# Optimization experiments

Hardware: AMD Instinct MI355X
Metric: run time of the kernel (lower is better)

Reference implementation:

```python
import math
import jax, jax.numpy as jnp
import numpy as np

B, L, D, K = 4, 1024, 256, 64
PI = np.float32(math.pi)


def setup_inputs() -> dict:
    key = jax.random.key(0)
    ks = jax.random.split(key, 16)
    s = 0.05
    return {
        "x": jax.random.normal(ks[0], (B, L, D), jnp.float32),
        "pos_phases": jax.random.normal(ks[1], (L, K), jnp.float32) * PI,
        "W1": jax.random.normal(ks[2], (D, D), jnp.float32) * s,
        "b1": jnp.zeros((D,), jnp.float32),
        "W2": jax.random.normal(ks[3], (D, K), jnp.float32) * s,
        "b2": jnp.zeros((K,), jnp.float32),
        "Wa": jax.random.normal(ks[4], (D, K), jnp.float32) * s,
        "ba": jnp.zeros((K,), jnp.float32),
        "Wv": jax.random.normal(ks[5], (D, D), jnp.float32) * s,
        "bv": jnp.zeros((D,), jnp.float32),
        "ln_g": jnp.ones((D,), jnp.float32),
        "ln_b": jnp.zeros((D,), jnp.float32),
        "Wo": jax.random.normal(ks[6], (D, D), jnp.float32) * s,
        "bo": jnp.zeros((D,), jnp.float32),
    }


def reference(x, pos_phases, W1, b1, W2, b2, Wa, ba, Wv, bv, ln_g, ln_b, Wo, bo):
    b, l, d = x.shape
    k = Wa.shape[1]
    # content phase encoder: Linear -> GELU(exact) -> Linear, then tanh * pi
    h = jax.nn.gelu(x @ W1 + b1, approximate=False)
    content_phase = jnp.tanh(h @ W2 + b2) * PI                      # (B,L,K)
    phase = pos_phases[None, :l] + content_phase                    # (B,L,K)
    amp = jax.nn.softplus(x @ Wa + ba) + 0.1                        # (B,L,K)
    # phasor = amp * exp(i*phase), kept as real/imag parts
    pr = amp * jnp.cos(phase)
    pim = amp * jnp.sin(phase)
    V = x @ Wv + bv                                                 # (B,L,D)
    # bound = phasor[...,None] * V[...,None,:]; cumsum over L
    mr = jnp.cumsum(pr[..., None] * V[..., None, :], axis=1)        # (B,L,K,D)
    mi = jnp.cumsum(pim[..., None] * V[..., None, :], axis=1)       # (B,L,K,D)
    # Re(memory * conj(phasor)) summed over K
    retrieved = (jnp.einsum('blkd,blk->bld', mr, pr)
                 + jnp.einsum('blkd,blk->bld', mi, pim))            # (B,L,D)
    positions = jnp.arange(1, l + 1, dtype=x.dtype)
    norm = jnp.sqrt(positions * k)[None, :, None]
    r = retrieved / norm
    # to_out: LayerNorm then Linear
    mu = jnp.mean(r, axis=-1, keepdims=True)
    var = jnp.var(r, axis=-1, keepdims=True)
    rn = (r - mu) * jax.lax.rsqrt(var + 1e-5) * ln_g + ln_b
    return x + (rn @ Wo + bo)
```

## Files before the change

### kernel.cpp

```cpp
#include <hip/hip_runtime.h>
#include <hip/hip_bf16.h>
#include <math.h>

#define BB 4
#define LL 1024
#define DD 256
#define KK 64
#define NN (BB*LL)

typedef __attribute__((ext_vector_type(8))) short short8;
typedef __attribute__((ext_vector_type(4))) float f32x4;

__device__ __forceinline__ short f2bs(float f){
    union { __hip_bfloat16 h; short s; } u;
    u.h = __float2bfloat16(f);
    return u.s;
}

__global__ __launch_bounds__(256)
void prep_kernel(const float* __restrict__ x,
                 const float* __restrict__ W1, const float* __restrict__ Wv,
                 const float* __restrict__ Wo, const float* __restrict__ W2,
                 const float* __restrict__ Wa,
                 short* __restrict__ xb,
                 short* __restrict__ W1t, short* __restrict__ Wvt,
                 short* __restrict__ Wot, short* __restrict__ W2t,
                 short* __restrict__ Wat)
{
    int o = blockIdx.x * 256 + threadIdx.x;
    if (o < NN*DD){
        xb[o] = f2bs(x[o]);
        return;
    }
    o -= NN*DD;
    if (o < 3*DD*DD){
        int m = o / (DD*DD);
        int e = o - m*DD*DD;
        int n = e >> 8, k = e & 255;
        const float* src = (m==0) ? W1 : (m==1) ? Wv : Wo;
        short* dst = (m==0) ? W1t : (m==1) ? Wvt : Wot;
        dst[n*DD + k] = f2bs(src[k*DD + n]);
        return;
    }
    o -= 3*DD*DD;
    int m = o >> 14;
    int e = o & 16383;
    int n = e >> 8, k = e & 255;
    const float* src = (m==0) ? W2 : Wa;
    short* dst = (m==0) ? W2t : Wat;
    dst[n*DD + k] = f2bs(src[k*KK + n]);
}

__global__ __launch_bounds__(256)
void encode_kernel(const short* __restrict__ xb, const float* __restrict__ pos,
                   const short* __restrict__ W1t, const short* __restrict__ Wvt,
                   const short* __restrict__ W2t, const short* __restrict__ Wat,
                   const float* __restrict__ b1, const float* __restrict__ bv,
                   const float* __restrict__ b2, const float* __restrict__ ba,
                   short* __restrict__ Pb, short* __restrict__ Vb)
{
    const int t = threadIdx.x;
    const int w = t >> 6, lane = t & 63;
    const int m16 = lane & 15, quad = lane >> 4;
    const int tok0 = blockIdx.x * 16;

    __shared__ __align__(16) short hsb[16][264];

    short8 aX[8];
    {
        const short* xr = xb + (size_t)(tok0 + m16)*DD + quad*8;
        #pragma unroll
        for (int kk = 0; kk < 8; kk++) aX[kk] = *(const short8*)(xr + kk*32);
    }

    f32x4 accH[4], accV[4];
    #pragma unroll
    for (int i = 0; i < 4; i++){ accH[i] = (f32x4){0,0,0,0}; accV[i] = (f32x4){0,0,0,0}; }
    #pragma unroll
    for (int kk = 0; kk < 8; kk++){
        const short* p1 = W1t + (size_t)(w*64 + m16)*DD + kk*32 + quad*8;
        const short* pv = Wvt + (size_t)(w*64 + m16)*DD + kk*32 + quad*8;
        #pragma unroll
        for (int ns = 0; ns < 4; ns++){
            accH[ns] = __builtin_amdgcn_mfma_f32_16x16x32_bf16(
                           aX[kk], *(const short8*)(p1 + ns*16*DD), accH[ns], 0,0,0);
            accV[ns] = __builtin_amdgcn_mfma_f32_16x16x32_bf16(
                           aX[kk], *(const short8*)(pv + ns*16*DD), accV[ns], 0,0,0);
        }
    }
    #pragma unroll
    for (int ns = 0; ns < 4; ns++){
        int col = w*64 + ns*16 + m16;
        float bb1 = b1[col], bbv = bv[col];
        #pragma unroll
        for (int r2 = 0; r2 < 4; r2++){
            int row = quad*4 + r2;
            float hx = accH[ns][r2] + bb1;
            hsb[row][col] = f2bs(0.5f*hx*(1.0f + erff(hx*0.70710678118f)));
            Vb[(size_t)(tok0+row)*DD + col] = f2bs(accV[ns][r2] + bbv);
        }
    }
    __syncthreads();

    f32x4 accT = (f32x4){0,0,0,0}, accA = (f32x4){0,0,0,0};
    {
        const short* p2 = W2t + (size_t)(w*16 + m16)*DD + quad*8;
        const short* pa = Wat + (size_t)(w*16 + m16)*DD + quad*8;
        #pragma unroll
        for (int kk = 0; kk < 8; kk++){
            short8 aH = *(const short8*)&hsb[m16][kk*32 + quad*8];
            accT = __builtin_amdgcn_mfma_f32_16x16x32_bf16(
                       aH, *(const short8*)(p2 + kk*32), accT, 0,0,0);
            accA = __builtin_amdgcn_mfma_f32_16x16x32_bf16(
                       aX[kk], *(const short8*)(pa + kk*32), accA, 0,0,0);
        }
    }
    const int k = w*16 + m16;
    float bb2 = b2[k], bba = ba[k];
    const float PI_ = 3.14159265358979323846f;
    #pragma unroll
    for (int r2 = 0; r2 < 4; r2++){
        int tok = tok0 + quad*4 + r2;
        float cp = tanhf(accT[r2] + bb2) * PI_;
        float ph = cp + pos[(tok & (LL-1))*KK + k];
        float za = accA[r2] + bba;
        float amp = ((za > 20.f) ? za : log1pf(expf(za))) + 0.1f;
        float sn, cs;
        sincosf(ph, &sn, &cs);
        Pb[(size_t)tok*128 + k]      = f2bs(amp*cs);
        Pb[(size_t)tok*128 + 64 + k] = f2bs(amp*sn);
    }
}

__global__ __launch_bounds__(256)
void transpose_v(const short* __restrict__ Vb, short* __restrict__ Vt)
{
    int o  = blockIdx.x * 256 + threadIdx.x;
    int b  = o >> 15;
    int d  = (o >> 7) & 255;
    int l0 = (o & 127) << 3;
    const short* src = Vb + ((size_t)b*1024 + l0)*DD + d;
    short8 v;
    #pragma unroll
    for (int i = 0; i < 8; i++) v[i] = src[(size_t)i*DD];
    *(short8*)(Vt + (((size_t)b*256 + d) << 10) + l0) = v;
}

__global__ __launch_bounds__(256)
void mix_kernel(const short* __restrict__ Pb, const short* __restrict__ Vt,
                float* __restrict__ R)
{
    const int t    = threadIdx.x;
    const int bb   = blockIdx.x >> 4;
    const int T    = blockIdx.x & 15;
    const int l0   = T * 64;
    const int cs   = blockIdx.y * 256;
    const int w    = t >> 6;
    const int lane = t & 63;
    const int m16  = lane & 15;
    const int quad = lane >> 4;
    const int mrow0 = l0 + w*16;
    const int lmaxw = mrow0 + 15;
    if (cs > lmaxw) return;

    __shared__ __align__(16) short sS[4][16][72];

    f32x4 accO[16];
    #pragma unroll
    for (int i = 0; i < 16; i++) accO[i] = (f32x4){0.f,0.f,0.f,0.f};

    const short* PbB = Pb + (size_t)bb * 1024 * 128;
    const short* VtB = Vt + (size_t)bb * 256 * 1024;

    short8 aP[4];
    {
        const short* ar = PbB + (size_t)(mrow0 + m16) * 128 + quad*8;
        #pragma unroll
        for (int kk = 0; kk < 4; kk++) aP[kk] = *(const short8*)(ar + kk*32);
    }

    const int cend = min(cs + 192, lmaxw);
    for (int c0 = cs; c0 <= cend; c0 += 64){
        f32x4 accS[4];
        #pragma unroll
        for (int i = 0; i < 4; i++) accS[i] = (f32x4){0.f,0.f,0.f,0.f};
        #pragma unroll
        for (int ns = 0; ns < 4; ns++){
            const short* br = PbB + (size_t)(c0 + ns*16 + m16) * 128 + quad*8;
            #pragma unroll
            for (int kk = 0; kk < 4; kk++){
                short8 bP = *(const short8*)(br + kk*32);
                accS[ns] = __builtin_amdgcn_mfma_f32_16x16x32_bf16(
                               aP[kk], bP, accS[ns], 0, 0, 0);
            }
        }
        #pragma unroll
        for (int ns = 0; ns < 4; ns++){
            int ccol = c0 + ns*16 + m16;
            #pragma unroll
            for (int r2 = 0; r2 < 4; r2++){
                int rrow = mrow0 + quad*4 + r2;
                float v = (ccol <= rrow) ? accS[ns][r2] : 0.f;
                sS[w][quad*4 + r2][ns*16 + m16] = f2bs(v);
            }
        }
        short8 aS0 = *(const short8*)&sS[w][m16][quad*8];
        short8 aS1 = *(const short8*)&sS[w][m16][32 + quad*8];
        #pragma unroll
        for (int ns = 0; ns < 16; ns++){
            const short* vr = VtB + (size_t)(ns*16 + m16) * 1024 + c0 + quad*8;
            short8 b0 = *(const short8*)(vr);
            short8 b1v = *(const short8*)(vr + 32);
            accO[ns] = __builtin_amdgcn_mfma_f32_16x16x32_bf16(
                           aS0, b0, accO[ns], 0, 0, 0);
            accO[ns] = __builtin_amdgcn_mfma_f32_16x16x32_bf16(
                           aS1, b1v, accO[ns], 0, 0, 0);
        }
    }

    float* Rb = R + (size_t)bb * 1024 * 256;
    #pragma unroll
    for (int ns = 0; ns < 16; ns++){
        #pragma unroll
        for (int r2 = 0; r2 < 4; r2++){
            int rrow = mrow0 + quad*4 + r2;
            atomicAdd(&Rb[(size_t)rrow*256 + ns*16 + m16], accO[ns][r2]);
        }
    }
}

__global__ __launch_bounds__(256)
void out_kernel(const float* __restrict__ R, const float* __restrict__ x,
                const float* __restrict__ ln_g, const float* __restrict__ ln_b,
                const short* __restrict__ Wot, const float* __restrict__ bo,
                float* __restrict__ out)
{
    const int t = threadIdx.x;
    const int w = t >> 6, lane = t & 63;
    const int m16 = lane & 15, quad = lane >> 4;
    const int tok0 = blockIdx.x * 16;

    __shared__ float rs[16][DD];
    __shared__ __align__(16) short rnb[16][264];
    __shared__ float stats[16][2];

    for (int i = t; i < 16*DD; i += 256){
        int r = i >> 8;
        int l = (tok0 + r) & (LL-1);
        rs[r][i&255] = R[(size_t)tok0*DD + i] * rsqrtf((float)(l+1) * (float)KK);
    }
    __syncthreads();

    #pragma unroll
    for (int rr = 0; rr < 4; rr++){
        int r = w*4 + rr;
        float s = 0.f, ss = 0.f;
        #pragma unroll
        for (int q = 0; q < 4; q++){
            float v = rs[r][q*64 + lane];
            s += v; ss += v*v;
        }
        for (int off = 32; off; off >>= 1){
            s  += __shfl_down(s, off);
            ss += __shfl_down(ss, off);
        }
        if (lane == 0){
            float mu = s * (1.0f/DD);
            float var = ss * (1.0f/DD) - mu*mu;
            stats[r][0] = mu;
            stats[r][1] = rsqrtf(var + 1e-5f);
        }
    }
    __syncthreads();

    for (int i = t; i < 16*DD; i += 256){
        int r = i >> 8, c = i & 255;
        rnb[r][c] = f2bs((rs[r][c] - stats[r][0]) * stats[r][1] * ln_g[c] + ln_b[c]);
    }
    __syncthreads();

    f32x4 acc[4];
    #pragma unroll
    for (int i = 0; i < 4; i++) acc[i] = (f32x4){0,0,0,0};
    #pragma unroll
    for (int kk = 0; kk < 8; kk++){
        short8 aR = *(const short8*)&rnb[m16][kk*32 + quad*8];
        const short* po = Wot + (size_t)(w*64 + m16)*DD + kk*32 + quad*8;
        #pragma unroll
        for (int ns = 0; ns < 4; ns++)
            acc[ns] = __builtin_amdgcn_mfma_f32_16x16x32_bf16(
                          aR, *(const short8*)(po + ns*16*DD), acc[ns], 0,0,0);
    }
    #pragma unroll
    for (int ns = 0; ns < 4; ns++){
        int col = w*64 + ns*16 + m16;
        float bbo = bo[col];
        #pragma unroll
        for (int r2 = 0; r2 < 4; r2++){
            size_t idx = (size_t)(tok0 + quad*4 + r2)*DD + col;
            out[idx] = x[idx] + acc[ns][r2] + bbo;
        }
    }
}

extern "C" void kernel_launch(void* const* d_in, const int* in_sizes, int n_in,
                              void* d_out, int out_size, void* d_ws, size_t ws_size,
                              hipStream_t stream) {
    const float* x    = (const float*)d_in[0];
    const float* pos  = (const float*)d_in[1];
    const float* W1   = (const float*)d_in[2];
    const float* b1   = (const float*)d_in[3];
    const float* W2   = (const float*)d_in[4];
    const float* b2_  = (const float*)d_in[5];
    const float* Wa   = (const float*)d_in[6];
    const float* ba   = (const float*)d_in[7];
    const float* Wv   = (const float*)d_in[8];
    const float* bv   = (const float*)d_in[9];
    const float* ln_g = (const float*)d_in[10];
    const float* ln_b = (const float*)d_in[11];
    const float* Wo   = (const float*)d_in[12];
    const float* bo   = (const float*)d_in[13];

    float* R   = (float*)d_ws;
    short* Pb  = (short*)(R + (size_t)NN*DD);
    short* Vb  = Pb  + (size_t)NN*128;
    short* Vt  = Vb  + (size_t)NN*256;
    short* xb  = Vt  + (size_t)NN*256;
    short* W1t = xb  + (size_t)NN*256;
    short* Wvt = W1t + DD*DD;
    short* Wot = Wvt + DD*DD;
    short* W2t = Wot + DD*DD;
    short* Wat = W2t + KK*DD;

    hipMemsetAsync(R, 0, (size_t)NN*DD*sizeof(float), stream);

    const int prep_n = NN*DD + 3*DD*DD + 2*KK*DD;
    prep_kernel<<<(prep_n + 255)/256, 256, 0, stream>>>(
        x, W1, Wv, Wo, W2, Wa, xb, W1t, Wvt, Wot, W2t, Wat);

    encode_kernel<<<NN/16, 256, 0, stream>>>(xb, pos, W1t, Wvt, W2t, Wat,
                                             b1, bv, b2_, ba, Pb, Vb);
    transpose_v<<<512, 256, 0, stream>>>(Vb, Vt);
    dim3 mixgrid(BB*16, 4);
    mix_kernel<<<mixgrid, 256, 0, stream>>>(Pb, Vt, R);
    out_kernel<<<NN/16, 256, 0, stream>>>(R, x, ln_g, ln_b, Wot, bo,
                                          (float*)d_out);
}
```

Before: 150.4 us.

## Fuse V transpose into encoder and replace atomics with per-split partial buffers

The encoder now stages V in shared memory and writes it directly in transposed layout, so the separate transpose kernel and the intermediate Vb buffer go away. The mix kernel splits the causal column range into 8 chunks of 128 instead of 4 of 256, for more parallel blocks. Each chunk writes plain stores into its own partial buffer instead of using atomicAdd on a zeroed R, which also removes the memset. The output kernel sums only the partials that can be non-zero for each token, at the cost of 8x more workspace and extra reads of the partials.

```diff
diff --git a/kernel.cpp b/kernel.cpp
--- a/kernel.cpp
+++ b/kernel.cpp
@@ -57,14 +57,17 @@
                    const short* __restrict__ W2t, const short* __restrict__ Wat,
                    const float* __restrict__ b1, const float* __restrict__ bv,
                    const float* __restrict__ b2, const float* __restrict__ ba,
-                   short* __restrict__ Pb, short* __restrict__ Vb)
+                   short* __restrict__ Pb, short* __restrict__ Vt)
 {
     const int t = threadIdx.x;
     const int w = t >> 6, lane = t & 63;
     const int m16 = lane & 15, quad = lane >> 4;
     const int tok0 = blockIdx.x * 16;
+    const int bsel = tok0 >> 10;
+    const int l0   = tok0 & 1023;
 
     __shared__ __align__(16) short hsb[16][264];
+    __shared__ __align__(16) short vsb[16][264];
 
     short8 aX[8];
     {
@@ -97,10 +100,21 @@
             int row = quad*4 + r2;
             float hx = accH[ns][r2] + bb1;
             hsb[row][col] = f2bs(0.5f*hx*(1.0f + erff(hx*0.70710678118f)));
-            Vb[(size_t)(tok0+row)*DD + col] = f2bs(accV[ns][r2] + bbv);
+            vsb[row][col] = f2bs(accV[ns][r2] + bbv);
         }
     }
     __syncthreads();
+
+    {
+        short8 v0, v1;
+        #pragma unroll
+        for (int r = 0; r < 8; r++) v0[r] = vsb[r][t];
+        #pragma unroll
+        for (int r = 0; r < 8; r++) v1[r] = vsb[8+r][t];
+        short* dst = Vt + (((size_t)bsel*256 + t) << 10) + l0;
+        *(short8*)dst = v0;
+        *(short8*)(dst + 8) = v1;
+    }
 
     f32x4 accT = (f32x4){0,0,0,0}, accA = (f32x4){0,0,0,0};
     {
@@ -133,28 +147,14 @@
 }
 
 __global__ __launch_bounds__(256)
-void transpose_v(const short* __restrict__ Vb, short* __restrict__ Vt)
-{
-    int o  = blockIdx.x * 256 + threadIdx.x;
-    int b  = o >> 15;
-    int d  = (o >> 7) & 255;
-    int l0 = (o & 127) << 3;
-    const short* src = Vb + ((size_t)b*1024 + l0)*DD + d;
-    short8 v;
-    #pragma unroll
-    for (int i = 0; i < 8; i++) v[i] = src[(size_t)i*DD];
-    *(short8*)(Vt + (((size_t)b*256 + d) << 10) + l0) = v;
-}
-
-__global__ __launch_bounds__(256)
 void mix_kernel(const short* __restrict__ Pb, const short* __restrict__ Vt,
-                float* __restrict__ R)
+                float* __restrict__ Rp)
 {
     const int t    = threadIdx.x;
     const int bb   = blockIdx.x >> 4;
     const int T    = blockIdx.x & 15;
     const int l0   = T * 64;
-    const int cs   = blockIdx.y * 256;
+    const int cs   = blockIdx.y * 128;
     const int w    = t >> 6;
     const int lane = t & 63;
     const int m16  = lane & 15;
@@ -179,7 +179,7 @@
         for (int kk = 0; kk < 4; kk++) aP[kk] = *(const short8*)(ar + kk*32);
     }
 
-    const int cend = min(cs + 192, lmaxw);
+    const int cend = min(cs + 64, lmaxw);
     for (int c0 = cs; c0 <= cend; c0 += 64){
         f32x4 accS[4];
         #pragma unroll
@@ -218,19 +218,19 @@
         }
     }
 
-    float* Rb = R + (size_t)bb * 1024 * 256;
+    float* Rw = Rp + (size_t)blockIdx.y * NN * DD + (size_t)bb * 1024 * 256;
     #pragma unroll
     for (int ns = 0; ns < 16; ns++){
         #pragma unroll
         for (int r2 = 0; r2 < 4; r2++){
             int rrow = mrow0 + quad*4 + r2;
-            atomicAdd(&Rb[(size_t)rrow*256 + ns*16 + m16], accO[ns][r2]);
+            Rw[(size_t)rrow*256 + ns*16 + m16] = accO[ns][r2];
         }
     }
 }
 
 __global__ __launch_bounds__(256)
-void out_kernel(const float* __restrict__ R, const float* __restrict__ x,
+void out_kernel(const float* __restrict__ Rp, const float* __restrict__ x,
                 const float* __restrict__ ln_g, const float* __restrict__ ln_b,
                 const short* __restrict__ Wot, const float* __restrict__ bo,
                 float* __restrict__ out)
@@ -239,6 +239,7 @@
     const int w = t >> 6, lane = t & 63;
     const int m16 = lane & 15, quad = lane >> 4;
     const int tok0 = blockIdx.x * 16;
+    const int pmax = (tok0 & 1023) >> 7;
 
     __shared__ float rs[16][DD];
     __shared__ __align__(16) short rnb[16][264];
@@ -247,7 +248,10 @@
     for (int i = t; i < 16*DD; i += 256){
         int r = i >> 8;
         int l = (tok0 + r) & (LL-1);
-        rs[r][i&255] = R[(size_t)tok0*DD + i] * rsqrtf((float)(l+1) * (float)KK);
+        float s = 0.f;
+        for (int p = 0; p <= pmax; p++)
+            s += Rp[(size_t)p*NN*DD + (size_t)tok0*DD + i];
+        rs[r][i&255] = s * rsqrtf((float)(l+1) * (float)KK);
     }
     __syncthreads();
 
@@ -321,10 +325,9 @@
     const float* Wo   = (const float*)d_in[12];
     const float* bo   = (const float*)d_in[13];
 
-    float* R   = (float*)d_ws;
-    short* Pb  = (short*)(R + (size_t)NN*DD);
-    short* Vb  = Pb  + (size_t)NN*128;
-    short* Vt  = Vb  + (size_t)NN*256;
+    float* Rp  = (float*)d_ws;
+    short* Pb  = (short*)(Rp + (size_t)8*NN*DD);
+    short* Vt  = Pb  + (size_t)NN*128;
     short* xb  = Vt  + (size_t)NN*256;
     short* W1t = xb  + (size_t)NN*256;
     short* Wvt = W1t + DD*DD;
@@ -332,17 +335,14 @@
     short* W2t = Wot + DD*DD;
     short* Wat = W2t + KK*DD;
 
-    hipMemsetAsync(R, 0, (size_t)NN*DD*sizeof(float), stream);
-
     const int prep_n = NN*DD + 3*DD*DD + 2*KK*DD;
     prep_kernel<<<(prep_n + 255)/256, 256, 0, stream>>>(
         x, W1, Wv, Wo, W2, Wa, xb, W1t, Wvt, Wot, W2t, Wat);
 
     encode_kernel<<<NN/16, 256, 0, stream>>>(xb, pos, W1t, Wvt, W2t, Wat,
-                                             b1, bv, b2_, ba, Pb, Vb);
-    transpose_v<<<512, 256, 0, stream>>>(Vb, Vt);
-    dim3 mixgrid(BB*16, 4);
-    mix_kernel<<<mixgrid, 256, 0, stream>>>(Pb, Vt, R);
-    out_kernel<<<NN/16, 256, 0, stream>>>(R, x, ln_g, ln_b, Wot, bo,
+                                             b1, bv, b2_, ba, Pb, Vt);
+    dim3 mixgrid(BB*16, 8);
+    mix_kernel<<<mixgrid, 256, 0, stream>>>(Pb, Vt, Rp);
+    out_kernel<<<NN/16, 256, 0, stream>>>(Rp, x, ln_g, ln_b, Wot, bo,
                                           (float*)d_out);
 }
```

After: 167.5 us. 1.11x slower.
